# Performance work log

Hardware: AMD Instinct MI355X
Metric: run time of the kernel (lower is better)

The kernel has to match this reference:

```python
import jax, jax.numpy as jnp
import numpy as np

LN_EPS = 1e-5


def setup_inputs() -> dict:
    key = jax.random.key(0)
    ks = jax.random.split(key, 6)
    B, S, D = 4, 4096, 2048
    Db = D // 4  # bottleneck_dim = n_embd // compression_ratio
    hidden = jax.random.normal(ks[0], (B, S, D), dtype=jnp.float32)
    # LayerNorm params (torch defaults: gamma=1, beta=0)
    ln_gamma = jnp.ones((D,), dtype=jnp.float32)
    ln_beta = jnp.zeros((D,), dtype=jnp.float32)
    # Linear weights, torch default init: U(-1/sqrt(fan_in), 1/sqrt(fan_in))
    bd_lim = 1.0 / np.sqrt(D)
    W_down = jax.random.uniform(ks[1], (D, Db), minval=-bd_lim, maxval=bd_lim, dtype=jnp.float32)
    b_down = jax.random.uniform(ks[2], (Db,), minval=-bd_lim, maxval=bd_lim, dtype=jnp.float32)
    bu_lim = 1.0 / np.sqrt(Db)
    W_up = jax.random.uniform(ks[3], (Db, D), minval=-bu_lim, maxval=bu_lim, dtype=jnp.float32)
    b_up = jax.random.uniform(ks[4], (D,), minval=-bu_lim, maxval=bu_lim, dtype=jnp.float32)
    alpha = jnp.array(0.01, dtype=jnp.float32)
    return {
        "hidden": hidden,
        "ln_gamma": ln_gamma,
        "ln_beta": ln_beta,
        "W_down": W_down,
        "b_down": b_down,
        "W_up": W_up,
        "b_up": b_up,
        "alpha": alpha,
        "layer_idx": 0,
    }


def reference(hidden, ln_gamma, ln_beta, W_down, b_down, W_up, b_up, alpha, layer_idx):
    # LayerNorm over last dim
    mu = jnp.mean(hidden, axis=-1, keepdims=True)
    var = jnp.mean(jnp.square(hidden - mu), axis=-1, keepdims=True)
    h_norm = (hidden - mu) * jax.lax.rsqrt(var + LN_EPS) * ln_gamma + ln_beta
    # down-proj -> SiLU -> up-proj   [b s d] @ [d k] -> [b s k] -> [b s d]
    z = jnp.einsum("bsd,dk->bsk", h_norm, W_down) + b_down
    z = jax.nn.silu(z)
    bottleneck_out = jnp.einsum("bsk,kd->bsd", z, W_up) + b_up
    # alpha-gated residual
    return hidden + alpha * (bottleneck_out - hidden)
```

## Files before the change

### kernel.cpp

```cpp
#include <hip/hip_runtime.h>

typedef __bf16 bf16x8 __attribute__((ext_vector_type(8)));
typedef __bf16 bf16x4 __attribute__((ext_vector_type(4)));
typedef float f32x4 __attribute__((ext_vector_type(4)));

#define S_BARRIER() asm volatile("s_barrier" ::: "memory")
#define WAITCNT_VM(n) asm volatile("s_waitcnt vmcnt(" #n ")" ::: "memory")
#define WAITCNT_LGKM0() asm volatile("s_waitcnt lgkmcnt(0)" ::: "memory")

__global__ __launch_bounds__(256) void prep_ln_kernel(
    const float* __restrict__ Wd, __bf16* __restrict__ Wtd,
    const float* __restrict__ Wu, __bf16* __restrict__ Wtu,
    const float* __restrict__ x, const float* __restrict__ g,
    const float* __restrict__ be, __bf16* __restrict__ y,
    int D, int Db, int ntiles) {
    if ((int)blockIdx.x < ntiles) {
        const float* W;
        __bf16* Wt;
        int K, N, tile;
        const int ntile_d = (Db / 32) * (D / 32);
        if ((int)blockIdx.x < ntile_d) {
            W = Wd; Wt = Wtd; K = D; N = Db; tile = blockIdx.x;
        } else {
            W = Wu; Wt = Wtu; K = Db; N = D; tile = blockIdx.x - ntile_d;
        }
        const int tn = tile % (N / 32), tk = tile / (N / 32);
        const int n0 = tn * 32, k0 = tk * 32;
        __shared__ float t[32][33];
        const int c = threadIdx.x & 31, r0 = threadIdx.x >> 5;
#pragma unroll
        for (int r = r0; r < 32; r += 8)
            t[r][c] = W[(size_t)(k0 + r) * N + n0 + c];
        __syncthreads();
#pragma unroll
        for (int r = r0; r < 32; r += 8)
            Wt[(size_t)(n0 + r) * K + k0 + c] = (__bf16)t[c][r];
        return;
    }
    const int t = threadIdx.x;
    const int wv = t >> 6, ln = t & 63;
    const size_t row = (size_t)(blockIdx.x - ntiles) * 4 + wv;
    const float4* xr = (const float4*)(x + row * (size_t)D);
    const int nv = D >> 3;
    float4 xs[16];
    float s = 0.f, ss = 0.f;
#pragma unroll
    for (int ii = 0; ii < 8; ++ii) {
        const int i = ii * 64 + ln;
        if (i < nv) {
            float4 v0 = xr[i * 2], v1 = xr[i * 2 + 1];
            xs[2 * ii] = v0;
            xs[2 * ii + 1] = v1;
            s += v0.x + v0.y + v0.z + v0.w + v1.x + v1.y + v1.z + v1.w;
            ss += v0.x * v0.x + v0.y * v0.y + v0.z * v0.z + v0.w * v0.w +
                  v1.x * v1.x + v1.y * v1.y + v1.z * v1.z + v1.w * v1.w;
        }
    }
#pragma unroll
    for (int o = 32; o > 0; o >>= 1) {
        s += __shfl_xor(s, o);
        ss += __shfl_xor(ss, o);
    }
    const float mu = s / (float)D;
    const float rstd = rsqrtf(ss / (float)D - mu * mu + 1e-5f);
    const float4* gg = (const float4*)g;
    const float4* bb = (const float4*)be;
    bf16x8* yr = (bf16x8*)(y + row * (size_t)D);
#pragma unroll
    for (int ii = 0; ii < 8; ++ii) {
        const int i = ii * 64 + ln;
        if (i < nv) {
            float4 v0 = xs[2 * ii], v1 = xs[2 * ii + 1];
            float4 g0 = gg[i * 2], g1 = gg[i * 2 + 1];
            float4 b0 = bb[i * 2], b1 = bb[i * 2 + 1];
            bf16x8 o;
            o[0] = (__bf16)((v0.x - mu) * rstd * g0.x + b0.x);
            o[1] = (__bf16)((v0.y - mu) * rstd * g0.y + b0.y);
            o[2] = (__bf16)((v0.z - mu) * rstd * g0.z + b0.z);
            o[3] = (__bf16)((v0.w - mu) * rstd * g0.w + b0.w);
            o[4] = (__bf16)((v1.x - mu) * rstd * g1.x + b1.x);
            o[5] = (__bf16)((v1.y - mu) * rstd * g1.y + b1.y);
            o[6] = (__bf16)((v1.z - mu) * rstd * g1.z + b1.z);
            o[7] = (__bf16)((v1.w - mu) * rstd * g1.w + b1.w);
            yr[i] = o;
        }
    }
}

template <int EPI, int BM, int BN, int MINW>
__global__ __launch_bounds__(256, MINW) void gemm_bt(
    const __bf16* __restrict__ A, const __bf16* __restrict__ Bt,
    const float* __restrict__ bias, const float* __restrict__ hid,
    const float* __restrict__ alpha_p, void* __restrict__ Cout,
    int M, int N, int K) {
    constexpr int BK = 32;
    constexpr int WM = BM / 2, WN = BN / 2;
    constexpr int MI = WM / 16, NJ = WN / 16;
    constexpr int GA = BM / 64, GB = BN / 64;
    constexpr int L = GA + GB;
    __shared__ __align__(16) __bf16 Ads[2][BM * BK];
    __shared__ __align__(16) __bf16 Bds[2][BN * BK];

    const int tid = threadIdx.x;
    const int wave = tid >> 6;
    const int lane = tid & 63;
    const int bn = blockIdx.x, bm = blockIdx.y;
    const int row0 = bm * BM, col0 = bn * BN;
    const int wr = wave >> 1, wc = wave & 1;

    f32x4 acc[MI][NJ] = {};

    const __bf16* Ag = A + (size_t)row0 * K;
    const __bf16* Bg = Bt + (size_t)col0 * K;
    const int lrow = lane >> 2;
    const int lk = ((lane & 3) ^ (lrow & 3)) * 8;

    const int c = lane & 15;
    const int q = lane >> 4;

    auto stage = [&](int k0, int b) {
#pragma unroll
        for (int p = 0; p < GA; ++p) {
            const int r = wave * (16 * GA) + p * 16;
            __builtin_amdgcn_global_load_lds(
                (__attribute__((address_space(1))) void*)(Ag + (size_t)(r + lrow) * K + k0 + lk),
                (__attribute__((address_space(3))) void*)(&Ads[b][r * BK]),
                16, 0, 0);
        }
#pragma unroll
        for (int p = 0; p < GB; ++p) {
            const int r = wave * (16 * GB) + p * 16;
            __builtin_amdgcn_global_load_lds(
                (__attribute__((address_space(1))) void*)(Bg + (size_t)(r + lrow) * K + k0 + lk),
                (__attribute__((address_space(3))) void*)(&Bds[b][r * BK]),
                16, 0, 0);
        }
    };

    const int nk = K / BK;
    stage(0, 0);
    for (int it = 0; it < nk; ++it) {
        const int cur = it & 1;
        if (it + 1 < nk) {
            stage((it + 1) * BK, cur ^ 1);
            if constexpr (L == 3) WAITCNT_VM(3); else WAITCNT_VM(4);
        } else {
            WAITCNT_VM(0);
        }
        S_BARRIER();

        bf16x8 afW[NJ], bfA[MI];
#pragma unroll
        for (int j = 0; j < NJ; ++j) {
            const int rl = wc * WN + j * 16 + c;
            afW[j] = *(const bf16x8*)(&Bds[cur][rl * BK + ((q ^ (c & 3)) * 8)]);
        }
#pragma unroll
        for (int i = 0; i < MI; ++i) {
            const int rl = wr * WM + i * 16 + c;
            bfA[i] = *(const bf16x8*)(&Ads[cur][rl * BK + ((q ^ (c & 3)) * 8)]);
        }
#pragma unroll
        for (int i = 0; i < MI; ++i)
#pragma unroll
            for (int j = 0; j < NJ; ++j)
                acc[i][j] = __builtin_amdgcn_mfma_f32_16x16x32_bf16(afW[j], bfA[i],
                                                                    acc[i][j], 0, 0, 0);
        WAITCNT_LGKM0();
        S_BARRIER();
    }

    float alpha = (EPI == 1) ? *alpha_p : 0.f;
#pragma unroll
    for (int i = 0; i < MI; ++i) {
        const int rowg = row0 + wr * WM + i * 16 + c;
        if (EPI == 0) {
#pragma unroll
            for (int j = 0; j < NJ; ++j) {
                const int colb = col0 + wc * WN + j * 16 + q * 4;
                const float4 bv = *(const float4*)(bias + colb);
                float v0 = acc[i][j][0] + bv.x;
                float v1 = acc[i][j][1] + bv.y;
                float v2 = acc[i][j][2] + bv.z;
                float v3 = acc[i][j][3] + bv.w;
                const size_t idx = (size_t)rowg * N + colb;
                bf16x4 o;
                o[0] = (__bf16)(v0 / (1.f + __expf(-v0)));
                o[1] = (__bf16)(v1 / (1.f + __expf(-v1)));
                o[2] = (__bf16)(v2 / (1.f + __expf(-v2)));
                o[3] = (__bf16)(v3 / (1.f + __expf(-v3)));
                *(bf16x4*)((__bf16*)Cout + idx) = o;
            }
        } else {
            float4 hv[NJ];
#pragma unroll
            for (int j = 0; j < NJ; ++j) {
                const int colb = col0 + wc * WN + j * 16 + q * 4;
                hv[j] = *(const float4*)(hid + (size_t)rowg * N + colb);
            }
#pragma unroll
            for (int j = 0; j < NJ; ++j) {
                const int colb = col0 + wc * WN + j * 16 + q * 4;
                const float4 bv = *(const float4*)(bias + colb);
                float v0 = acc[i][j][0] + bv.x;
                float v1 = acc[i][j][1] + bv.y;
                float v2 = acc[i][j][2] + bv.z;
                float v3 = acc[i][j][3] + bv.w;
                float4 o;
                o.x = hv[j].x + alpha * (v0 - hv[j].x);
                o.y = hv[j].y + alpha * (v1 - hv[j].y);
                o.z = hv[j].z + alpha * (v2 - hv[j].z);
                o.w = hv[j].w + alpha * (v3 - hv[j].w);
                *(float4*)((float*)Cout + (size_t)rowg * N + colb) = o;
            }
        }
    }
}

extern "C" void kernel_launch(void* const* d_in, const int* in_sizes, int n_in,
                              void* d_out, int out_size, void* d_ws, size_t ws_size,
                              hipStream_t stream) {
    const float* hidden = (const float*)d_in[0];
    const float* ln_gamma = (const float*)d_in[1];
    const float* ln_beta = (const float*)d_in[2];
    const float* W_down = (const float*)d_in[3];
    const float* b_down = (const float*)d_in[4];
    const float* W_up = (const float*)d_in[5];
    const float* b_up = (const float*)d_in[6];
    const float* alpha = (const float*)d_in[7];
    float* out = (float*)d_out;

    const int D = in_sizes[2];
    const int Db = in_sizes[4];
    const int M = in_sizes[0] / D;

    char* w = (char*)d_ws;
    __bf16* hn = (__bf16*)w;  w += (size_t)M * D * sizeof(__bf16);
    __bf16* z = (__bf16*)w;   w += (size_t)M * Db * sizeof(__bf16);
    __bf16* Wtd = (__bf16*)w; w += (size_t)D * Db * sizeof(__bf16);
    __bf16* Wtu = (__bf16*)w; w += (size_t)Db * D * sizeof(__bf16);

    const int ntiles = 2 * (D / 32) * (Db / 32);
    prep_ln_kernel<<<ntiles + M / 4, 256, 0, stream>>>(W_down, Wtd, W_up, Wtu,
                                                       hidden, ln_gamma, ln_beta, hn,
                                                       D, Db, ntiles);

    gemm_bt<0, 64, 128, 5><<<dim3(Db / 128, M / 64), 256, 0, stream>>>(
        hn, Wtd, b_down, nullptr, nullptr, (void*)z, M, Db, D);

    gemm_bt<1, 128, 128, 4><<<dim3(D / 128, M / 128), 256, 0, stream>>>(
        z, Wtu, b_up, hidden, alpha, (void*)out, M, D, Db);
}
```

Baseline: 392.6 us.

## Fuse LayerNorm into down-projection GEMM via folded gamma/beta and post-scaling

Removes the separate LayerNorm pass and its bf16 normalized-activation buffer. The down-proj GEMM now reads fp32 hidden directly, converts it to bf16 in LDS, and accumulates per-row sums and sums of squares on the way. Normalization is applied algebraically in the epilogue as rstd*acc - mu*rstd*C1 + C2, where C1 and C2 are per-column weight sums precomputed with atomics in the weight-prep kernel, and gamma is folded into the bf16 weights. This drops one full M×D write and read but makes the GEMM read fp32 A, which doubles A traffic per tile and is no longer double-buffered. It also applies the bf16 rounding before mean subtraction, which adds error when the mean is large.

```diff
diff --git a/kernel.cpp b/kernel.cpp
--- a/kernel.cpp
+++ b/kernel.cpp
@@ -8,81 +8,179 @@
 #define WAITCNT_VM(n) asm volatile("s_waitcnt vmcnt(" #n ")" ::: "memory")
 #define WAITCNT_LGKM0() asm volatile("s_waitcnt lgkmcnt(0)" ::: "memory")
 
-__global__ __launch_bounds__(256) void prep_ln_kernel(
+__global__ __launch_bounds__(256) void prep_w_kernel(
     const float* __restrict__ Wd, __bf16* __restrict__ Wtd,
     const float* __restrict__ Wu, __bf16* __restrict__ Wtu,
-    const float* __restrict__ x, const float* __restrict__ g,
-    const float* __restrict__ be, __bf16* __restrict__ y,
-    int D, int Db, int ntiles) {
-    if ((int)blockIdx.x < ntiles) {
-        const float* W;
-        __bf16* Wt;
-        int K, N, tile;
-        const int ntile_d = (Db / 32) * (D / 32);
-        if ((int)blockIdx.x < ntile_d) {
-            W = Wd; Wt = Wtd; K = D; N = Db; tile = blockIdx.x;
-        } else {
-            W = Wu; Wt = Wtu; K = Db; N = D; tile = blockIdx.x - ntile_d;
-        }
+    const float* __restrict__ g, const float* __restrict__ be,
+    float* __restrict__ C1, float* __restrict__ C2b,
+    int D, int Db) {
+    const int ntile_d = (Db / 32) * (D / 32);
+    __shared__ float t[32][33];
+    const int c = threadIdx.x & 31, r0 = threadIdx.x >> 5;
+    if ((int)blockIdx.x < ntile_d) {
+        const int K = D, N = Db, tile = blockIdx.x;
         const int tn = tile % (N / 32), tk = tile / (N / 32);
         const int n0 = tn * 32, k0 = tk * 32;
-        __shared__ float t[32][33];
-        const int c = threadIdx.x & 31, r0 = threadIdx.x >> 5;
 #pragma unroll
         for (int r = r0; r < 32; r += 8)
-            t[r][c] = W[(size_t)(k0 + r) * N + n0 + c];
+            t[r][c] = Wd[(size_t)(k0 + r) * N + n0 + c];
         __syncthreads();
+        const float gv = g[k0 + c];
+        const float bv = be[k0 + c];
+        float c1p[4], c2p[4];
+#pragma unroll
+        for (int u = 0; u < 4; ++u) {
+            const int r = r0 + u * 8;
+            const float wv = t[c][r];
+            const __bf16 w16 = (__bf16)(gv * wv);
+            Wtd[(size_t)(n0 + r) * K + k0 + c] = w16;
+            c1p[u] = (float)w16;
+            c2p[u] = bv * wv;
+        }
+#pragma unroll
+        for (int o = 16; o > 0; o >>= 1)
+#pragma unroll
+            for (int u = 0; u < 4; ++u) {
+                c1p[u] += __shfl_xor(c1p[u], o);
+                c2p[u] += __shfl_xor(c2p[u], o);
+            }
+        if (c == 0)
+#pragma unroll
+            for (int u = 0; u < 4; ++u) {
+                atomicAdd(&C1[n0 + r0 + u * 8], c1p[u]);
+                atomicAdd(&C2b[n0 + r0 + u * 8], c2p[u]);
+            }
+    } else {
+        const int K = Db, N = D, tile = blockIdx.x - ntile_d;
+        const int tn = tile % (N / 32), tk = tile / (N / 32);
+        const int n0 = tn * 32, k0 = tk * 32;
 #pragma unroll
         for (int r = r0; r < 32; r += 8)
-            Wt[(size_t)(n0 + r) * K + k0 + c] = (__bf16)t[c][r];
-        return;
-    }
-    const int t = threadIdx.x;
-    const int wv = t >> 6, ln = t & 63;
-    const size_t row = (size_t)(blockIdx.x - ntiles) * 4 + wv;
-    const float4* xr = (const float4*)(x + row * (size_t)D);
-    const int nv = D >> 3;
-    float4 xs[16];
+            t[r][c] = Wu[(size_t)(k0 + r) * N + n0 + c];
+        __syncthreads();
+#pragma unroll
+        for (int r = r0; r < 32; r += 8)
+            Wtu[(size_t)(n0 + r) * K + k0 + c] = (__bf16)t[c][r];
+    }
+}
+
+__global__ __launch_bounds__(256, 4) void fused_ln_down(
+    const float* __restrict__ X, const __bf16* __restrict__ Bt,
+    const float* __restrict__ C1, const float* __restrict__ C2b,
+    __bf16* __restrict__ Z, int M, int N, int K) {
+    constexpr int BM = 64, BN = 128, BK = 32;
+    constexpr int WM = 32, WN = 64, MI = 2, NJ = 4;
+    __shared__ __align__(16) __bf16 Ads[BM * BK];
+    __shared__ __align__(16) __bf16 Bds[2][BN * BK];
+    __shared__ float sRow[BM], ssRow[BM];
+
+    const int tid = threadIdx.x;
+    const int wave = tid >> 6, lane = tid & 63;
+    const int bn = blockIdx.x, bm = blockIdx.y;
+    const int row0 = bm * BM, col0 = bn * BN;
+    const int wr = wave >> 1, wc = wave & 1;
+
+    f32x4 acc[MI][NJ] = {};
+
+    const int lrow = lane >> 2;
+    const int chunk = (lane & 3) ^ (lrow & 3);
+    const int arow = wave * 16 + lrow;
+    const float* Axr = X + (size_t)(row0 + arow) * K + chunk * 8;
+    const __bf16* Bg = Bt + (size_t)col0 * K;
+    const int lk = chunk * 8;
+
+    const int c = lane & 15, q = lane >> 4;
+
+    auto stageB = [&](int k0, int b) {
+#pragma unroll
+        for (int p = 0; p < 2; ++p) {
+            const int r = wave * 32 + p * 16;
+            __builtin_amdgcn_global_load_lds(
+                (__attribute__((address_space(1))) void*)(Bg + (size_t)(r + lrow) * K + k0 + lk),
+                (__attribute__((address_space(3))) void*)(&Bds[b][r * BK]),
+                16, 0, 0);
+        }
+    };
+
     float s = 0.f, ss = 0.f;
-#pragma unroll
-    for (int ii = 0; ii < 8; ++ii) {
-        const int i = ii * 64 + ln;
-        if (i < nv) {
-            float4 v0 = xr[i * 2], v1 = xr[i * 2 + 1];
-            xs[2 * ii] = v0;
-            xs[2 * ii + 1] = v1;
-            s += v0.x + v0.y + v0.z + v0.w + v1.x + v1.y + v1.z + v1.w;
-            ss += v0.x * v0.x + v0.y * v0.y + v0.z * v0.z + v0.w * v0.w +
-                  v1.x * v1.x + v1.y * v1.y + v1.z * v1.z + v1.w * v1.w;
-        }
-    }
-#pragma unroll
-    for (int o = 32; o > 0; o >>= 1) {
-        s += __shfl_xor(s, o);
-        ss += __shfl_xor(ss, o);
-    }
-    const float mu = s / (float)D;
-    const float rstd = rsqrtf(ss / (float)D - mu * mu + 1e-5f);
-    const float4* gg = (const float4*)g;
-    const float4* bb = (const float4*)be;
-    bf16x8* yr = (bf16x8*)(y + row * (size_t)D);
-#pragma unroll
-    for (int ii = 0; ii < 8; ++ii) {
-        const int i = ii * 64 + ln;
-        if (i < nv) {
-            float4 v0 = xs[2 * ii], v1 = xs[2 * ii + 1];
-            float4 g0 = gg[i * 2], g1 = gg[i * 2 + 1];
-            float4 b0 = bb[i * 2], b1 = bb[i * 2 + 1];
-            bf16x8 o;
-            o[0] = (__bf16)((v0.x - mu) * rstd * g0.x + b0.x);
-            o[1] = (__bf16)((v0.y - mu) * rstd * g0.y + b0.y);
-            o[2] = (__bf16)((v0.z - mu) * rstd * g0.z + b0.z);
-            o[3] = (__bf16)((v0.w - mu) * rstd * g0.w + b0.w);
-            o[4] = (__bf16)((v1.x - mu) * rstd * g1.x + b1.x);
-            o[5] = (__bf16)((v1.y - mu) * rstd * g1.y + b1.y);
-            o[6] = (__bf16)((v1.z - mu) * rstd * g1.z + b1.z);
-            o[7] = (__bf16)((v1.w - mu) * rstd * g1.w + b1.w);
-            yr[i] = o;
+    const int nk = K / BK;
+    stageB(0, 0);
+    float4 a0 = *(const float4*)(Axr);
+    float4 a1 = *(const float4*)(Axr + 4);
+    for (int it = 0; it < nk; ++it) {
+        const int cur = it & 1;
+        float4 n0, n1;
+        if (it + 1 < nk) {
+            stageB((it + 1) * BK, cur ^ 1);
+            n0 = *(const float4*)(Axr + (it + 1) * BK);
+            n1 = *(const float4*)(Axr + (it + 1) * BK + 4);
+            WAITCNT_VM(4);
+        } else {
+            WAITCNT_VM(0);
+        }
+        s += a0.x + a0.y + a0.z + a0.w + a1.x + a1.y + a1.z + a1.w;
+        ss += a0.x * a0.x + a0.y * a0.y + a0.z * a0.z + a0.w * a0.w +
+              a1.x * a1.x + a1.y * a1.y + a1.z * a1.z + a1.w * a1.w;
+        bf16x8 av;
+        av[0] = (__bf16)a0.x; av[1] = (__bf16)a0.y;
+        av[2] = (__bf16)a0.z; av[3] = (__bf16)a0.w;
+        av[4] = (__bf16)a1.x; av[5] = (__bf16)a1.y;
+        av[6] = (__bf16)a1.z; av[7] = (__bf16)a1.w;
+        *(bf16x8*)(&Ads[arow * BK + (lane & 3) * 8]) = av;
+        WAITCNT_LGKM0();
+        S_BARRIER();
+
+        bf16x8 afW[NJ], bfA[MI];
+#pragma unroll
+        for (int j = 0; j < NJ; ++j) {
+            const int rl = wc * WN + j * 16 + c;
+            afW[j] = *(const bf16x8*)(&Bds[cur][rl * BK + ((q ^ (c & 3)) * 8)]);
+        }
+#pragma unroll
+        for (int i = 0; i < MI; ++i) {
+            const int rl = wr * WM + i * 16 + c;
+            bfA[i] = *(const bf16x8*)(&Ads[rl * BK + ((q ^ (c & 3)) * 8)]);
+        }
+#pragma unroll
+        for (int i = 0; i < MI; ++i)
+#pragma unroll
+            for (int j = 0; j < NJ; ++j)
+                acc[i][j] = __builtin_amdgcn_mfma_f32_16x16x32_bf16(afW[j], bfA[i],
+                                                                    acc[i][j], 0, 0, 0);
+        WAITCNT_LGKM0();
+        S_BARRIER();
+        a0 = n0; a1 = n1;
+    }
+
+    s += __shfl_xor(s, 1);  s += __shfl_xor(s, 2);
+    ss += __shfl_xor(ss, 1); ss += __shfl_xor(ss, 2);
+    if ((lane & 3) == 0) { sRow[arow] = s; ssRow[arow] = ss; }
+    __syncthreads();
+
+    const float rK = 1.f / (float)K;
+#pragma unroll
+    for (int i = 0; i < MI; ++i) {
+        const int rl = wr * WM + i * 16 + c;
+        const float mu = sRow[rl] * rK;
+        const float var = ssRow[rl] * rK - mu * mu;
+        const float rstd = rsqrtf(var + 1e-5f);
+        const float mrs = mu * rstd;
+        const int rowg = row0 + rl;
+#pragma unroll
+        for (int j = 0; j < NJ; ++j) {
+            const int colb = col0 + wc * WN + j * 16 + q * 4;
+            const float4 c1 = *(const float4*)(C1 + colb);
+            const float4 c2 = *(const float4*)(C2b + colb);
+            float v0 = rstd * acc[i][j][0] - mrs * c1.x + c2.x;
+            float v1 = rstd * acc[i][j][1] - mrs * c1.y + c2.y;
+            float v2 = rstd * acc[i][j][2] - mrs * c1.z + c2.z;
+            float v3 = rstd * acc[i][j][3] - mrs * c1.w + c2.w;
+            bf16x4 o;
+            o[0] = (__bf16)(v0 / (1.f + __expf(-v0)));
+            o[1] = (__bf16)(v1 / (1.f + __expf(-v1)));
+            o[2] = (__bf16)(v2 / (1.f + __expf(-v2)));
+            o[3] = (__bf16)(v3 / (1.f + __expf(-v3)));
+            *(bf16x4*)(Z + (size_t)rowg * N + colb) = o;
         }
     }
 }
@@ -235,18 +333,21 @@
     const int M = in_sizes[0] / D;
 
     char* w = (char*)d_ws;
-    __bf16* hn = (__bf16*)w;  w += (size_t)M * D * sizeof(__bf16);
     __bf16* z = (__bf16*)w;   w += (size_t)M * Db * sizeof(__bf16);
     __bf16* Wtd = (__bf16*)w; w += (size_t)D * Db * sizeof(__bf16);
     __bf16* Wtu = (__bf16*)w; w += (size_t)Db * D * sizeof(__bf16);
+    float* C1 = (float*)w;    w += Db * sizeof(float);
+    float* C2b = (float*)w;   w += Db * sizeof(float);
+
+    hipMemsetAsync(C1, 0, Db * sizeof(float), stream);
+    hipMemcpyAsync(C2b, b_down, Db * sizeof(float), hipMemcpyDeviceToDevice, stream);
 
     const int ntiles = 2 * (D / 32) * (Db / 32);
-    prep_ln_kernel<<<ntiles + M / 4, 256, 0, stream>>>(W_down, Wtd, W_up, Wtu,
-                                                       hidden, ln_gamma, ln_beta, hn,
-                                                       D, Db, ntiles);
-
-    gemm_bt<0, 64, 128, 5><<<dim3(Db / 128, M / 64), 256, 0, stream>>>(
-        hn, Wtd, b_down, nullptr, nullptr, (void*)z, M, Db, D);
+    prep_w_kernel<<<ntiles, 256, 0, stream>>>(W_down, Wtd, W_up, Wtu,
+                                              ln_gamma, ln_beta, C1, C2b, D, Db);
+
+    fused_ln_down<<<dim3(Db / 128, M / 64), 256, 0, stream>>>(
+        hidden, Wtd, C1, C2b, z, M, Db, D);
 
     gemm_bt<1, 128, 128, 4><<<dim3(D / 128, M / 128), 256, 0, stream>>>(
         z, Wtu, b_up, hidden, alpha, (void*)out, M, D, Db);
```

Result: slower. 406.8 us (+3.6%).
